# Performance work log

Measured on AMD Instinct MI355X. Metric: run time of the kernel, lower is better.

## Reference

```python
import jax, jax.numpy as jnp
import numpy as np

D = 256      # model_dim
H = 4        # num_heads
DPH = D // H # dim_per_head = 64
NLBL = 9     # number of per-label linear layers


def setup_inputs() -> dict:
    key0 = jax.random.key(0)
    ks = jax.random.split(key0, 16)
    N, M = 6144, 6144
    s = 1.0 / np.sqrt(D)
    inp = {
        'key':     jax.random.normal(ks[0], (N, D), jnp.float32),
        'value':   jax.random.normal(ks[1], (N, D), jnp.float32),
        'query':   jax.random.normal(ks[2], (M, D), jnp.float32),
        'label_1': jax.random.randint(ks[3], (N,), 0, NLBL),
        'label_2': jax.random.randint(ks[4], (M,), 0, NLBL),
        # 9 per-label projection weights (applied as x @ W + b)
        'Wq': jax.random.normal(ks[5], (NLBL, D, D), jnp.float32) * s,
        'bq': jax.random.normal(ks[6], (NLBL, D), jnp.float32) * 0.02,
        'Wk': jax.random.normal(ks[7], (NLBL, D, D), jnp.float32) * s,
        'bk': jax.random.normal(ks[8], (NLBL, D), jnp.float32) * 0.02,
        'Wv': jax.random.normal(ks[9], (NLBL, D, D), jnp.float32) * s,
        'bv': jax.random.normal(ks[10], (NLBL, D), jnp.float32) * 0.02,
        'Wf': jax.random.normal(ks[11], (D, D), jnp.float32) * s,
        'bf': jax.random.normal(ks[12], (D,), jnp.float32) * 0.02,
        'gamma': jnp.ones((D,), jnp.float32),
        'beta':  jnp.zeros((D,), jnp.float32),
    }
    return inp


def _label_proj(x, W, b, lbl):
    # Project every token with all 9 label weights, then pick the per-token one.
    # p: [n, 9, D]
    p = jnp.einsum('nd,ldo->nlo', x, W) + b[None]
    return jnp.take_along_axis(p, lbl[:, None, None], axis=1)[:, 0]  # [n, D]


def reference(key, value, query, label_1, label_2,
              Wq, bq, Wk, bk, Wv, bv, Wf, bf, gamma, beta):
    M = query.shape[0]
    # Per-label (dynamically routed) projections; within a group the query
    # label equals the key label, so per-token weight selection is exactly
    # the per-group loop of the original module.
    q = _label_proj(query, Wq, bq, label_2).reshape(M, H, DPH)
    k = _label_proj(key,   Wk, bk, label_1).reshape(-1, H, DPH)
    v = _label_proj(value, Wv, bv, label_1).reshape(-1, H, DPH)

    # Note: original uses scale = (dim_per_head // num_heads) ** -0.5
    scale = (DPH // H) ** (-0.5)
    scores = jnp.einsum('mhd,nhd->hmn', q, k) * scale  # [H, M, N]

    # Queries only attend to keys of the same label (block structure of
    # the original per-label gather/attention/scatter loop).
    mask = label_2[:, None] == label_1[None, :]        # [M, N]
    probs = jax.nn.softmax(jnp.where(mask[None], scores, -1e30), axis=-1)

    ctx = jnp.einsum('hmn,nhd->mhd', probs, v).reshape(M, D)
    out = ctx @ Wf + bf
    res = query + out  # residual is the unprojected query

    mu = jnp.mean(res, axis=-1, keepdims=True)
    var = jnp.var(res, axis=-1, keepdims=True)
    return (res - mu) / jnp.sqrt(var + 1e-5) * gamma + beta
```

## Files before the change

kernel.cpp:

```cpp
#include <hip/hip_runtime.h>
#include <hip/hip_bf16.h>

#define D 256
#define H 4
#define DPH 64
#define NLBL 9
#define SPLITK 4

typedef __attribute__((ext_vector_type(8))) __bf16 bf16x8;
typedef __attribute__((ext_vector_type(8))) unsigned short u16x8;
typedef __attribute__((ext_vector_type(4))) float f32x4;

__device__ __forceinline__ int sw_idx(int row, int col) {
  return row * 64 + (col ^ ((row & 7) << 3));
}

__device__ __forceinline__ unsigned int pk2(float a, float b) {
  unsigned int lo = (unsigned int)__builtin_bit_cast(unsigned short, (__bf16)a);
  unsigned int hi = (unsigned int)__builtin_bit_cast(unsigned short, (__bf16)b);
  return lo | (hi << 16);
}

__device__ __forceinline__ float b2f(unsigned short u) {
  return __builtin_bit_cast(float, (unsigned int)u << 16);
}

__device__ __forceinline__ bf16x8 cvt8(float4 u0, float4 u1) {
  bf16x8 r;
  r[0] = (__bf16)u0.x; r[1] = (__bf16)u0.y; r[2] = (__bf16)u0.z; r[3] = (__bf16)u0.w;
  r[4] = (__bf16)u1.x; r[5] = (__bf16)u1.y; r[6] = (__bf16)u1.z; r[7] = (__bf16)u1.w;
  return r;
}

__global__ __launch_bounds__(1024) void prep_kernel(
    const int* __restrict__ lbl1, int n1, const int* __restrict__ lbl2, int n2,
    const float* __restrict__ Wq, const float* __restrict__ Wk,
    const float* __restrict__ Wv, const float* __restrict__ Wf,
    __bf16* __restrict__ Wqt, __bf16* __restrict__ Wkt,
    __bf16* __restrict__ Wvt, __bf16* __restrict__ Wft,
    int* __restrict__ cnt, int* __restrict__ off,
    int* __restrict__ pqo, int* __restrict__ pko,
    int* __restrict__ tq, int* __restrict__ tk, int* __restrict__ ntl,
    int* __restrict__ korder, int* __restrict__ qorder) {
  const int job = blockIdx.x;
  const int t = threadIdx.x, lane = t & 63, wave = t >> 6;

  __shared__ int bins[2 * NLBL];
  __shared__ int wtot[16];
  __shared__ float tlds[64][65];

  if (job < 18) {
    const int l = job % NLBL, a = job / NLBL;
    const int n = a ? n2 : n1;
    const int* lbl = a ? lbl2 : lbl1;
    int* order = a ? qorder : korder;

    if (t < NLBL) bins[t] = 0;
    __syncthreads();
    for (int chunk = 0; chunk < n; chunk += 1024) {
      int i = chunk + t;
      int lb = (i < n) ? lbl[i] : -1;
#pragma unroll
      for (int lab = 0; lab < NLBL; ++lab) {
        unsigned long long bal = __ballot(lb == lab);
        if (lane == 0 && bal) atomicAdd(&bins[lab], __popcll(bal));
      }
    }
    __syncthreads();
    int base = 0;
#pragma unroll
    for (int i = 0; i < NLBL; ++i) base += (i < l) ? bins[i] : 0;

    int pos = 0;
    for (int chunk = 0; chunk < n; chunk += 1024) {
      int i = chunk + t;
      bool flag = (i < n) && (lbl[i] == l);
      unsigned long long bal = __ballot(flag);
      int wprefix = __popcll(bal & ((1ull << lane) - 1ull));
      if (lane == 0) wtot[wave] = __popcll(bal);
      __syncthreads();
      int prew = 0, tot = 0;
#pragma unroll
      for (int w = 0; w < 16; ++w) {
        prew += (w < wave) ? wtot[w] : 0;
        tot += wtot[w];
      }
      if (flag) order[base + pos + prew + wprefix] = i;
      pos += tot;
      __syncthreads();
    }
    return;
  }

  if (job == 18) {
    if (t < 2 * NLBL) bins[t] = 0;
    __syncthreads();
    for (int a = 0; a < 2; ++a) {
      const int n = a ? n2 : n1;
      const int* lbl = a ? lbl2 : lbl1;
      for (int chunk = 0; chunk < n; chunk += 1024) {
        int i = chunk + t;
        int lb = (i < n) ? lbl[i] : -1;
#pragma unroll
        for (int lab = 0; lab < NLBL; ++lab) {
          unsigned long long bal = __ballot(lb == lab);
          if (lane == 0 && bal) atomicAdd(&bins[a * NLBL + lab], __popcll(bal));
        }
      }
    }
    __syncthreads();
    if (t < 2 * NLBL) cnt[t] = bins[t];
    if (t == 0) {
      int a0 = 0, a1 = 0, p0 = 0, p1 = 0, t0 = 0, t1 = 0;
      for (int l = 0; l < NLBL; ++l) {
        off[l] = a0;      a0 += bins[l];
        off[10 + l] = a1; a1 += bins[NLBL + l];
        pko[l] = p0; pqo[l] = p1;
        int tkl = (bins[l] + 63) >> 6;
        int tql = (bins[NLBL + l] + 127) >> 7;
        for (int i = 0; i < tkl; ++i) { tk[2 * t0] = l; tk[2 * t0 + 1] = p0 + (i << 6); ++t0; }
        for (int i = 0; i < tql; ++i) { tq[2 * t1] = l; tq[2 * t1 + 1] = p1 + (i << 7); ++t1; }
        p0 += tkl << 6; p1 += tql << 7;
      }
      off[9] = a0; off[19] = a1; pko[9] = p0; pqo[9] = p1;
      ntl[0] = t1; ntl[1] = t0;
    }
    return;
  }

  {
    int j = job - 19;
    int m = j >> 4, sub = j & 15;
    const float* src; __bf16* dst;
    if (m < 9)       { src = Wq + (size_t)m * 65536;        dst = Wqt + (size_t)m * 65536; }
    else if (m < 18) { src = Wk + (size_t)(m - 9) * 65536;  dst = Wkt + (size_t)(m - 9) * 65536; }
    else if (m < 27) { src = Wv + (size_t)(m - 18) * 65536; dst = Wvt + (size_t)(m - 18) * 65536; }
    else             { src = Wf;                            dst = Wft; }
    int k0 = (sub >> 2) << 6, n0 = (sub & 3) << 6;
    int rr = t >> 6, c = t & 63;
#pragma unroll
    for (int i = 0; i < 4; ++i) {
      int r = i * 16 + rr;
      tlds[r][c] = src[(size_t)(k0 + r) * D + n0 + c];
    }
    __syncthreads();
#pragma unroll
    for (int i = 0; i < 4; ++i) {
      int r = i * 16 + rr;
      dst[(size_t)(n0 + r) * D + k0 + c] = (__bf16)tlds[c][r];
    }
  }
}

__global__ __launch_bounds__(256) void gemm_in_kernel(
    const float* __restrict__ query, const float* __restrict__ key,
    const float* __restrict__ value,
    const __bf16* __restrict__ Wqt, const __bf16* __restrict__ Wkt,
    const __bf16* __restrict__ Wvt,
    const float* __restrict__ bq, const float* __restrict__ bk,
    const float* __restrict__ bv,
    const int* __restrict__ qorder, const int* __restrict__ korder,
    const int* __restrict__ off, const int* __restrict__ cnt,
    const int* __restrict__ pqo, const int* __restrict__ pko,
    const int* __restrict__ tq, const int* __restrict__ tk,
    const int* __restrict__ ntl,
    __bf16* __restrict__ qbuf, __bf16* __restrict__ kbuf, __bf16* __restrict__ vbuf) {
  const int y = blockIdx.y;
  const int nt = (y == 0) ? ntl[0] : ntl[1];
  const int ti = (y == 0) ? ((int)blockIdx.x >> 2) : ((int)blockIdx.x >> 1);
  const int sub = (y == 0) ? ((int)blockIdx.x & 3) : ((int)blockIdx.x & 1);
  if (ti >= nt) return;
  const int* tt = (y == 0) ? tq : tk;
  const float* x = (y == 0) ? query : (y == 1 ? key : value);
  const __bf16* W = (y == 0) ? Wqt : (y == 1 ? Wkt : Wvt);
  const float* bias = (y == 0) ? bq : (y == 1 ? bk : bv);
  const int* order = (y == 0) ? qorder : korder;
  const int* po = (y == 0) ? pqo : pko;
  __bf16* outp = (y == 0) ? qbuf : (y == 1 ? kbuf : vbuf);
  const float sc = (y == 0) ? 0.36067376f : 1.0f;

  const int l = tt[2 * ti], prow0 = tt[2 * ti + 1] + sub * 32;
  const int cl = (y == 0) ? cnt[NLBL + l] : cnt[l];
  const int ooff = (y == 0) ? off[10 + l] : off[l];
  const int base = prow0 - po[l];

  const int t = threadIdx.x, w = t >> 6, lane = t & 63;
  const int lr = lane & 15, lk = lane >> 4;

  int src[2];
#pragma unroll
  for (int fi = 0; fi < 2; ++fi) {
    int ridx = base + fi * 16 + lr;
    src[fi] = (ridx < cl) ? order[ooff + ridx] : -1;
  }

  bf16x8 az;
#pragma unroll
  for (int j = 0; j < 8; ++j) az[j] = (__bf16)0.f;

  f32x4 acc[2][4];
#pragma unroll
  for (int i = 0; i < 2; ++i)
#pragma unroll
    for (int j = 0; j < 4; ++j) acc[i][j] = (f32x4){0.f, 0.f, 0.f, 0.f};

  for (int kb = 0; kb < 8; ++kb) {
    const int kbase = kb * 32 + lk * 8;
    bf16x8 a[2], b[4];
#pragma unroll
    for (int fi = 0; fi < 2; ++fi) {
      if (src[fi] >= 0) {
        const float* ap = x + (size_t)src[fi] * D + kbase;
        float4 u0 = *(const float4*)ap;
        float4 u1 = *(const float4*)(ap + 4);
        a[fi] = cvt8(u0, u1);
      } else {
        a[fi] = az;
      }
    }
#pragma unroll
    for (int fj = 0; fj < 4; ++fj) {
      int col = w * 64 + fj * 16 + lr;
      b[fj] = *(const bf16x8*)(W + (size_t)l * 65536 + (size_t)col * D + kbase);
    }
#pragma unroll
    for (int fi = 0; fi < 2; ++fi)
#pragma unroll
      for (int fj = 0; fj < 4; ++fj)
        acc[fi][fj] = __builtin_amdgcn_mfma_f32_16x16x32_bf16(a[fi], b[fj], acc[fi][fj], 0, 0, 0);
  }

#pragma unroll
  for (int fj = 0; fj < 4; ++fj) {
    int col = w * 64 + fj * 16 + lr;
    float bv_ = bias[l * D + col];
#pragma unroll
    for (int fi = 0; fi < 2; ++fi)
#pragma unroll
      for (int r = 0; r < 4; ++r) {
        int row = prow0 + fi * 16 + lk * 4 + r;
        outp[(size_t)row * D + col] = (__bf16)((acc[fi][fj][r] + bv_) * sc);
      }
  }
}

__global__ __launch_bounds__(256) void attn_mfma(
    const __bf16* __restrict__ qbuf, const __bf16* __restrict__ kbuf,
    const __bf16* __restrict__ vbuf, const int* __restrict__ cnt,
    const int* __restrict__ tq, const int* __restrict__ ntl,
    const int* __restrict__ pko,
    __bf16* __restrict__ pctx, float* __restrict__ pstats) {
  const int tqi = blockIdx.x;
  if (tqi >= ntl[0]) return;
  const int l = tq[2 * tqi], prow0 = tq[2 * tqi + 1];
  const int h = blockIdx.y, s = blockIdx.z;
  const int nk = cnt[l];
  const int ntiles = (nk + 63) >> 6;
  const int ntsz = (ntiles + SPLITK - 1) / SPLITK;
  const int tt0 = s * ntsz;
  const int tt1 = min(ntiles, tt0 + ntsz);
  if (tt0 >= tt1) return;

  const int t = threadIdx.x;
  const int w = t >> 6, lane = t & 63;
  const int lr = lane & 15, lk = lane >> 4;

  __shared__ __align__(16) unsigned short ks[4096];
  __shared__ __align__(16) unsigned short vtl[4096];
  __shared__ __align__(16) unsigned short plds[8192];

  const int qbase = prow0 + w * 32;
  bf16x8 b_q[2][2];
#pragma unroll
  for (int qf = 0; qf < 2; ++qf)
#pragma unroll
    for (int kb = 0; kb < 2; ++kb)
      b_q[qf][kb] = *(const bf16x8*)(qbuf + (size_t)(qbase + qf * 16 + lr) * D +
                                     h * DPH + kb * 32 + lk * 8);

  f32x4 acc_o[2][4];
#pragma unroll
  for (int qf = 0; qf < 2; ++qf)
#pragma unroll
    for (int i = 0; i < 4; ++i) acc_o[qf][i] = (f32x4){0.f, 0.f, 0.f, 0.f};
  float lrun[2] = {0.f, 0.f};
  const int kb0 = pko[l];

  const int krow = t >> 2, kc0 = (t & 3) * 16;
  const __bf16* kptr = kbuf + (size_t)(kb0 + krow) * D + h * DPH + kc0;
  const int vkey2 = (t & 31) * 2, vd0 = (t >> 5) * 8;
  const __bf16* vptr = vbuf + (size_t)(kb0 + vkey2) * D + h * DPH + vd0;

  uint4 kreg0, kreg1;
  u16x8 vreg0, vreg1;
  auto LOADT = [&](int tt) {
    const __bf16* kp = kptr + ((size_t)tt << 6) * D;
    kreg0 = *(const uint4*)kp;
    kreg1 = *(const uint4*)(kp + 8);
    const __bf16* vp = vptr + ((size_t)tt << 6) * D;
    vreg0 = *(const u16x8*)vp;
    vreg1 = *(const u16x8*)(vp + D);
  };

  LOADT(tt0);
  for (int tt = tt0; tt < tt1; ++tt) {
    const int n0 = tt << 6;
    __syncthreads();
    *(uint4*)&ks[sw_idx(krow, kc0)] = kreg0;
    *(uint4*)&ks[sw_idx(krow, kc0 + 8)] = kreg1;
#pragma unroll
    for (int j = 0; j < 8; ++j) {
      unsigned int u = (unsigned int)vreg0[j] | ((unsigned int)vreg1[j] << 16);
      *(unsigned int*)&vtl[sw_idx(vd0 + j, vkey2)] = u;
    }
    __syncthreads();
    if (tt + 1 < tt1) LOADT(tt + 1);

    f32x4 s_acc[2][4];
    const f32x4 zz = {0.f, 0.f, 0.f, 0.f};
#pragma unroll
    for (int fi = 0; fi < 4; ++fi) {
      bf16x8 a0 = *(const bf16x8*)&ks[sw_idx(fi * 16 + lr, lk * 8)];
#pragma unroll
      for (int qf = 0; qf < 2; ++qf)
        s_acc[qf][fi] = __builtin_amdgcn_mfma_f32_16x16x32_bf16(a0, b_q[qf][0], zz, 0, 0, 0);
    }
#pragma unroll
    for (int fi = 0; fi < 4; ++fi) {
      bf16x8 a1 = *(const bf16x8*)&ks[sw_idx(fi * 16 + lr, 32 + lk * 8)];
#pragma unroll
      for (int qf = 0; qf < 2; ++qf)
        s_acc[qf][fi] = __builtin_amdgcn_mfma_f32_16x16x32_bf16(a1, b_q[qf][1], s_acc[qf][fi], 0, 0, 0);
    }

    float p[2][16];
#pragma unroll
    for (int qf = 0; qf < 2; ++qf) {
      float ts = 0.f;
#pragma unroll
      for (int fi = 0; fi < 4; ++fi)
#pragma unroll
        for (int r = 0; r < 4; ++r) {
          int key = n0 + fi * 16 + lk * 4 + r;
          float pv = (key < nk) ? exp2f(s_acc[qf][fi][r]) : 0.f;
          p[qf][fi * 4 + r] = pv;
          ts += pv;
        }
      ts += __shfl_xor(ts, 16, 64);
      ts += __shfl_xor(ts, 32, 64);
      lrun[qf] += ts;
    }

#pragma unroll
    for (int qf = 0; qf < 2; ++qf)
#pragma unroll
      for (int fi = 0; fi < 4; ++fi) {
        unsigned int w0 = pk2(p[qf][fi * 4 + 0], p[qf][fi * 4 + 1]);
        unsigned int w1 = pk2(p[qf][fi * 4 + 2], p[qf][fi * 4 + 3]);
        int idx = w * 2048 + sw_idx(qf * 16 + lr, fi * 16 + lk * 4);
        *(uint2*)&plds[idx] = make_uint2(w0, w1);
      }

#pragma unroll
    for (int kb = 0; kb < 2; ++kb) {
      bf16x8 bp[2];
#pragma unroll
      for (int qf = 0; qf < 2; ++qf)
        bp[qf] = *(const bf16x8*)&plds[w * 2048 + sw_idx(qf * 16 + lr, kb * 32 + lk * 8)];
#pragma unroll
      for (int fi = 0; fi < 4; ++fi) {
        bf16x8 av = *(const bf16x8*)&vtl[sw_idx(fi * 16 + lr, kb * 32 + lk * 8)];
#pragma unroll
        for (int qf = 0; qf < 2; ++qf)
          acc_o[qf][fi] = __builtin_amdgcn_mfma_f32_16x16x32_bf16(av, bp[qf], acc_o[qf][fi], 0, 0, 0);
      }
    }
  }

  const size_t pbase = ((size_t)tqi * H + h) * SPLITK + s;
  __bf16* pc = pctx + pbase * 8192;
#pragma unroll
  for (int qf = 0; qf < 2; ++qf) {
    int qloc = w * 32 + qf * 16 + lr;
#pragma unroll
    for (int fi = 0; fi < 4; ++fi) {
      uint2 u;
      u.x = pk2(acc_o[qf][fi][0], acc_o[qf][fi][1]);
      u.y = pk2(acc_o[qf][fi][2], acc_o[qf][fi][3]);
      *(uint2*)(pc + qloc * 64 + fi * 16 + lk * 4) = u;
    }
    if (lk == 0) pstats[pbase * 128 + qloc] = lrun[qf];
  }
}

__global__ __launch_bounds__(256) void proj_ln_kernel(
    const __bf16* __restrict__ pctx, const float* __restrict__ pstats,
    const __bf16* __restrict__ Wft, const float* __restrict__ bf_,
    const float* __restrict__ query,
    const int* __restrict__ qorder, const int* __restrict__ off,
    const int* __restrict__ cnt, const int* __restrict__ pqo,
    const int* __restrict__ tq, const int* __restrict__ ntl,
    const float* __restrict__ gamma, const float* __restrict__ beta,
    float* __restrict__ out) {
  const int tqi = blockIdx.x;
  if (tqi >= ntl[0]) return;
  const int l = tq[2 * tqi];
  const int qq = blockIdx.y;
  const int prow0 = tq[2 * tqi + 1] + qq * 32;
  const int qloc0 = qq * 32;
  const int cl = cnt[NLBL + l];
  const int ooff = off[10 + l];
  const int base = prow0 - pqo[l];
  const int nk = cnt[l];
  const int ntiles = (nk + 63) >> 6;
  const int ntsz = (ntiles + SPLITK - 1) / SPLITK;
  const int nsp = ntiles ? (ntiles + ntsz - 1) / ntsz : 0;

  const int t = threadIdx.x, w = t >> 6, lane = t & 63;
  const int lr = lane & 15, lk = lane >> 4;

  __shared__ int srcs[32];
  __shared__ float linv[32][4];
  __shared__ __align__(16) unsigned short ct[32 * 256];
  __shared__ float psum[4][32], psum2[4][32];
  __shared__ float mu_s[32], is_s[32];

  if (t < 32) {
    int ridx = base + t;
    srcs[t] = (ridx < cl) ? qorder[ooff + ridx] : -1;
  }
  if (t < 128) {
    int row = t >> 2, h = t & 3;
    float L = 0.f;
    for (int s = 0; s < nsp; ++s)
      L += pstats[(((size_t)tqi * H + h) * SPLITK + s) * 128 + qloc0 + row];
    linv[row][h] = (L > 0.f) ? (1.f / L) : 0.f;
  }
  __syncthreads();

  {
    int row = t >> 3, dseg = (t & 7) * 32;
    int h = dseg >> 6, d0 = dseg & 63;
    const __bf16* pb = pctx + (((size_t)tqi * H + h) * SPLITK) * 8192 +
                       (size_t)(qloc0 + row) * 64 + d0;
    float v[32];
#pragma unroll
    for (int j = 0; j < 32; ++j) v[j] = 0.f;
    for (int s = 0; s < nsp; ++s) {
      const __bf16* ps = pb + (size_t)s * 8192;
#pragma unroll
      for (int j4 = 0; j4 < 4; ++j4) {
        u16x8 u = *(const u16x8*)(ps + j4 * 8);
#pragma unroll
        for (int e = 0; e < 8; ++e) v[j4 * 8 + e] += b2f(u[e]);
      }
    }
    float iv = linv[row][h];
    int xr = (row & 7) << 3;
#pragma unroll
    for (int j = 0; j < 32; j += 2)
      *(unsigned int*)&ct[row * 256 + ((dseg + j) ^ xr)] = pk2(v[j] * iv, v[j + 1] * iv);
  }
  __syncthreads();

  f32x4 acc[2][4];
#pragma unroll
  for (int i = 0; i < 2; ++i)
#pragma unroll
    for (int j = 0; j < 4; ++j) acc[i][j] = (f32x4){0.f, 0.f, 0.f, 0.f};

  for (int kb = 0; kb < 8; ++kb) {
    const int kbase = kb * 32 + lk * 8;
    bf16x8 a[2], b[4];
#pragma unroll
    for (int fi = 0; fi < 2; ++fi) {
      int row = fi * 16 + lr;
      a[fi] = *(const bf16x8*)&ct[row * 256 + (kbase ^ ((row & 7) << 3))];
    }
#pragma unroll
    for (int fj = 0; fj < 4; ++fj) {
      int col = w * 64 + fj * 16 + lr;
      b[fj] = *(const bf16x8*)(Wft + (size_t)col * D + kbase);
    }
#pragma unroll
    for (int fi = 0; fi < 2; ++fi)
#pragma unroll
      for (int fj = 0; fj < 4; ++fj)
        acc[fi][fj] = __builtin_amdgcn_mfma_f32_16x16x32_bf16(a[fi], b[fj], acc[fi][fj], 0, 0, 0);
  }

  float res[2][4][4];
  float s1[2][4], s2[2][4];
#pragma unroll
  for (int fi = 0; fi < 2; ++fi)
#pragma unroll
    for (int r = 0; r < 4; ++r) { s1[fi][r] = 0.f; s2[fi][r] = 0.f; }

#pragma unroll
  for (int fj = 0; fj < 4; ++fj) {
    int col = w * 64 + fj * 16 + lr;
    float bcol = bf_[col];
#pragma unroll
    for (int fi = 0; fi < 2; ++fi)
#pragma unroll
      for (int r = 0; r < 4; ++r) {
        int rowl = fi * 16 + lk * 4 + r;
        int sr = srcs[rowl];
        float qv = (sr >= 0) ? query[(size_t)sr * D + col] : 0.f;
        float v = acc[fi][fj][r] + bcol + qv;
        res[fi][fj][r] = v;
        s1[fi][r] += v;
        s2[fi][r] += v * v;
      }
  }

#pragma unroll
  for (int o2 = 1; o2 <= 8; o2 <<= 1) {
#pragma unroll
    for (int fi = 0; fi < 2; ++fi)
#pragma unroll
      for (int r = 0; r < 4; ++r) {
        s1[fi][r] += __shfl_xor(s1[fi][r], o2, 64);
        s2[fi][r] += __shfl_xor(s2[fi][r], o2, 64);
      }
  }
  if (lr == 0) {
#pragma unroll
    for (int fi = 0; fi < 2; ++fi)
#pragma unroll
      for (int r = 0; r < 4; ++r) {
        int rowl = fi * 16 + lk * 4 + r;
        psum[w][rowl] = s1[fi][r];
        psum2[w][rowl] = s2[fi][r];
      }
  }
  __syncthreads();
  if (t < 32) {
    float tot = psum[0][t] + psum[1][t] + psum[2][t] + psum[3][t];
    float tot2 = psum2[0][t] + psum2[1][t] + psum2[2][t] + psum2[3][t];
    float mu = tot * (1.f / D);
    float var = tot2 * (1.f / D) - mu * mu;
    mu_s[t] = mu;
    is_s[t] = rsqrtf(var + 1e-5f);
  }
  __syncthreads();

#pragma unroll
  for (int fj = 0; fj < 4; ++fj) {
    int col = w * 64 + fj * 16 + lr;
    float gc = gamma[col], bc = beta[col];
#pragma unroll
    for (int fi = 0; fi < 2; ++fi)
#pragma unroll
      for (int r = 0; r < 4; ++r) {
        int rowl = fi * 16 + lk * 4 + r;
        int sr = srcs[rowl];
        if (sr >= 0)
          out[(size_t)sr * D + col] =
              (res[fi][fj][r] - mu_s[rowl]) * is_s[rowl] * gc + bc;
      }
  }
}

extern "C" void kernel_launch(void* const* d_in, const int* in_sizes, int n_in,
                              void* d_out, int out_size, void* d_ws, size_t ws_size,
                              hipStream_t stream) {
  const float* key   = (const float*)d_in[0];
  const float* value = (const float*)d_in[1];
  const float* query = (const float*)d_in[2];
  const int*   lbl1  = (const int*)d_in[3];
  const int*   lbl2  = (const int*)d_in[4];
  const float* Wq = (const float*)d_in[5];
  const float* bq = (const float*)d_in[6];
  const float* Wk = (const float*)d_in[7];
  const float* bk = (const float*)d_in[8];
  const float* Wv = (const float*)d_in[9];
  const float* bv = (const float*)d_in[10];
  const float* Wf = (const float*)d_in[11];
  const float* bf_ = (const float*)d_in[12];
  const float* gamma = (const float*)d_in[13];
  const float* beta  = (const float*)d_in[14];
  float* out = (float*)d_out;

  const int N = in_sizes[0] / D;
  const int M = in_sizes[2] / D;
  const int MP = M + NLBL * 128;
  const int NP = N + NLBL * 64;
  const int TQCAP = (M + 127) / 128 + NLBL;
  const int TKCAP = (N + 63) / 64 + NLBL;

  int* cnt = (int*)d_ws;
  int* off = cnt + 32;
  int* pqo = off + 32;
  int* pko = pqo + 16;
  int* ntl = pko + 16;
  int* tq  = ntl + 16;
  int* tk  = tq + 2 * TQCAP;
  int* korder = tk + 2 * TKCAP;
  int* qorder = korder + N;
  size_t ihdr = (((size_t)(112 + 2 * TQCAP + 2 * TKCAP + N + M)) * 4 + 255) & ~(size_t)255;

  __bf16* Wqt = (__bf16*)((char*)d_ws + ihdr);
  __bf16* Wkt = Wqt + (size_t)9 * 65536;
  __bf16* Wvt = Wkt + (size_t)9 * 65536;
  __bf16* Wft = Wvt + (size_t)9 * 65536;
  __bf16* qbuf = Wft + 65536;
  __bf16* kbuf = qbuf + (size_t)MP * D;
  __bf16* vbuf = kbuf + (size_t)NP * D;
  __bf16* pctx = vbuf + (size_t)NP * D;
  float* pstats = (float*)(pctx + (size_t)TQCAP * H * SPLITK * 8192);

  prep_kernel<<<19 + 28 * 16, 1024, 0, stream>>>(
      lbl1, N, lbl2, M, Wq, Wk, Wv, Wf, Wqt, Wkt, Wvt, Wft,
      cnt, off, pqo, pko, tq, tk, ntl, korder, qorder);

  int gx = TQCAP * 4 > TKCAP * 2 ? TQCAP * 4 : TKCAP * 2;
  gemm_in_kernel<<<dim3(gx, 3), 256, 0, stream>>>(
      query, key, value, Wqt, Wkt, Wvt, bq, bk, bv,
      qorder, korder, off, cnt, pqo, pko, tq, tk, ntl, qbuf, kbuf, vbuf);

  attn_mfma<<<dim3(TQCAP, H, SPLITK), 256, 0, stream>>>(
      qbuf, kbuf, vbuf, cnt, tq, ntl, pko, pctx, pstats);

  proj_ln_kernel<<<dim3(TQCAP, 4), 256, 0, stream>>>(
      pctx, pstats, Wft, bf_, query, qorder, off, cnt, pqo, tq, ntl,
      gamma, beta, out);
}
```

Before: 88.92 us.

## Fuse four kernels into one persistent cooperative kernel with grid syncs

Merges the prep, input GEMM, attention and projection+LayerNorm kernels into a single persistent cooperative kernel. Blocks loop over jobs in each phase and phases are separated by grid-wide syncs. The per-kernel launch gaps go away and the grid is sized from occupancy. The prep phase now runs with 256-thread blocks instead of 1024, and shared memory is a union across phases. Grid syncs add overhead, and using fewer blocks than before may reduce parallelism in the attention phase.

```diff
diff --git a/kernel.cpp b/kernel.cpp
--- a/kernel.cpp
+++ b/kernel.cpp
@@ -1,11 +1,16 @@
 #include <hip/hip_runtime.h>
 #include <hip/hip_bf16.h>
+#include <hip/hip_cooperative_groups.h>
+
+namespace cg = cooperative_groups;
 
 #define D 256
 #define H 4
 #define DPH 64
 #define NLBL 9
 #define SPLITK 4
+#define GRID 512
+#define BLK 256
 
 typedef __attribute__((ext_vector_type(8))) __bf16 bf16x8;
 typedef __attribute__((ext_vector_type(8))) unsigned short u16x8;
@@ -32,60 +37,72 @@
   return r;
 }
 
-__global__ __launch_bounds__(1024) void prep_kernel(
-    const int* __restrict__ lbl1, int n1, const int* __restrict__ lbl2, int n2,
-    const float* __restrict__ Wq, const float* __restrict__ Wk,
-    const float* __restrict__ Wv, const float* __restrict__ Wf,
-    __bf16* __restrict__ Wqt, __bf16* __restrict__ Wkt,
-    __bf16* __restrict__ Wvt, __bf16* __restrict__ Wft,
-    int* __restrict__ cnt, int* __restrict__ off,
-    int* __restrict__ pqo, int* __restrict__ pko,
-    int* __restrict__ tq, int* __restrict__ tk, int* __restrict__ ntl,
-    int* __restrict__ korder, int* __restrict__ qorder) {
-  const int job = blockIdx.x;
+struct SMemSC { int bins[2 * NLBL]; int wtot[4]; };
+struct SMemAT { unsigned short ks[4096]; unsigned short vtl[4096]; unsigned short plds[8192]; };
+struct SMemPL {
+  int srcs[32]; float linv[32][4];
+  unsigned short ct[32 * 256];
+  float psum[4][32], psum2[4][32], mu_s[32], is_s[32];
+};
+union __align__(16) SMem {
+  SMemSC sc;
+  float tlds[64][65];
+  SMemAT at;
+  SMemPL pl;
+};
+
+struct P {
+  const float *key, *value, *query;
+  const int *lbl1, *lbl2;
+  const float *Wq, *bq, *Wk, *bk, *Wv, *bv, *Wf, *bf_, *gamma, *beta;
+  float* out;
+  int N, M;
+  int *cnt, *off, *pqo, *pko, *tq, *tk, *ntl, *korder, *qorder;
+  __bf16 *Wqt, *Wkt, *Wvt, *Wft, *qbuf, *kbuf, *vbuf, *pctx;
+  float* pstats;
+  int phase_lo, phase_hi;
+};
+
+__device__ void ph_prep(const P& p, SMem& sm, int job) {
   const int t = threadIdx.x, lane = t & 63, wave = t >> 6;
-
-  __shared__ int bins[2 * NLBL];
-  __shared__ int wtot[16];
-  __shared__ float tlds[64][65];
 
   if (job < 18) {
     const int l = job % NLBL, a = job / NLBL;
-    const int n = a ? n2 : n1;
-    const int* lbl = a ? lbl2 : lbl1;
-    int* order = a ? qorder : korder;
-
-    if (t < NLBL) bins[t] = 0;
+    const int n = a ? p.M : p.N;
+    const int* lbl = a ? p.lbl2 : p.lbl1;
+    int* order = a ? p.qorder : p.korder;
+
+    if (t < NLBL) sm.sc.bins[t] = 0;
     __syncthreads();
-    for (int chunk = 0; chunk < n; chunk += 1024) {
+    for (int chunk = 0; chunk < n; chunk += BLK) {
       int i = chunk + t;
       int lb = (i < n) ? lbl[i] : -1;
 #pragma unroll
       for (int lab = 0; lab < NLBL; ++lab) {
         unsigned long long bal = __ballot(lb == lab);
-        if (lane == 0 && bal) atomicAdd(&bins[lab], __popcll(bal));
+        if (lane == 0 && bal) atomicAdd(&sm.sc.bins[lab], __popcll(bal));
       }
     }
     __syncthreads();
     int base = 0;
 #pragma unroll
-    for (int i = 0; i < NLBL; ++i) base += (i < l) ? bins[i] : 0;
+    for (int i = 0; i < NLBL; ++i) base += (i < l) ? sm.sc.bins[i] : 0;
 
     int pos = 0;
-    for (int chunk = 0; chunk < n; chunk += 1024) {
+    for (int chunk = 0; chunk < n; chunk += BLK) {
       int i = chunk + t;
       bool flag = (i < n) && (lbl[i] == l);
       unsigned long long bal = __ballot(flag);
-      int wprefix = __popcll(bal & ((1ull << lane) - 1ull));
-      if (lane == 0) wtot[wave] = __popcll(bal);
+      int wpref = __popcll(bal & ((1ull << lane) - 1ull));
+      if (lane == 0) sm.sc.wtot[wave] = __popcll(bal);
       __syncthreads();
       int prew = 0, tot = 0;
 #pragma unroll
-      for (int w = 0; w < 16; ++w) {
-        prew += (w < wave) ? wtot[w] : 0;
-        tot += wtot[w];
-      }
-      if (flag) order[base + pos + prew + wprefix] = i;
+      for (int w = 0; w < 4; ++w) {
+        prew += (w < wave) ? sm.sc.wtot[w] : 0;
+        tot += sm.sc.wtot[w];
+      }
+      if (flag) order[base + pos + prew + wpref] = i;
       pos += tot;
       __syncthreads();
     }
@@ -93,37 +110,37 @@
   }
 
   if (job == 18) {
-    if (t < 2 * NLBL) bins[t] = 0;
+    if (t < 2 * NLBL) sm.sc.bins[t] = 0;
     __syncthreads();
     for (int a = 0; a < 2; ++a) {
-      const int n = a ? n2 : n1;
-      const int* lbl = a ? lbl2 : lbl1;
-      for (int chunk = 0; chunk < n; chunk += 1024) {
+      const int n = a ? p.M : p.N;
+      const int* lbl = a ? p.lbl2 : p.lbl1;
+      for (int chunk = 0; chunk < n; chunk += BLK) {
         int i = chunk + t;
         int lb = (i < n) ? lbl[i] : -1;
 #pragma unroll
         for (int lab = 0; lab < NLBL; ++lab) {
           unsigned long long bal = __ballot(lb == lab);
-          if (lane == 0 && bal) atomicAdd(&bins[a * NLBL + lab], __popcll(bal));
+          if (lane == 0 && bal) atomicAdd(&sm.sc.bins[a * NLBL + lab], __popcll(bal));
         }
       }
     }
     __syncthreads();
-    if (t < 2 * NLBL) cnt[t] = bins[t];
+    if (t < 2 * NLBL) p.cnt[t] = sm.sc.bins[t];
     if (t == 0) {
       int a0 = 0, a1 = 0, p0 = 0, p1 = 0, t0 = 0, t1 = 0;
       for (int l = 0; l < NLBL; ++l) {
-        off[l] = a0;      a0 += bins[l];
-        off[10 + l] = a1; a1 += bins[NLBL + l];
-        pko[l] = p0; pqo[l] = p1;
-        int tkl = (bins[l] + 63) >> 6;
-        int tql = (bins[NLBL + l] + 127) >> 7;
-        for (int i = 0; i < tkl; ++i) { tk[2 * t0] = l; tk[2 * t0 + 1] = p0 + (i << 6); ++t0; }
-        for (int i = 0; i < tql; ++i) { tq[2 * t1] = l; tq[2 * t1 + 1] = p1 + (i << 7); ++t1; }
+        p.off[l] = a0;      a0 += sm.sc.bins[l];
+        p.off[10 + l] = a1; a1 += sm.sc.bins[NLBL + l];
+        p.pko[l] = p0; p.pqo[l] = p1;
+        int tkl = (sm.sc.bins[l] + 63) >> 6;
+        int tql = (sm.sc.bins[NLBL + l] + 127) >> 7;
+        for (int i = 0; i < tkl; ++i) { p.tk[2 * t0] = l; p.tk[2 * t0 + 1] = p0 + (i << 6); ++t0; }
+        for (int i = 0; i < tql; ++i) { p.tq[2 * t1] = l; p.tq[2 * t1 + 1] = p1 + (i << 7); ++t1; }
         p0 += tkl << 6; p1 += tql << 7;
       }
-      off[9] = a0; off[19] = a1; pko[9] = p0; pqo[9] = p1;
-      ntl[0] = t1; ntl[1] = t0;
+      p.off[9] = a0; p.off[19] = a1; p.pko[9] = p0; p.pqo[9] = p1;
+      p.ntl[0] = t1; p.ntl[1] = t0;
     }
     return;
   }
@@ -132,56 +149,39 @@
     int j = job - 19;
     int m = j >> 4, sub = j & 15;
     const float* src; __bf16* dst;
-    if (m < 9)       { src = Wq + (size_t)m * 65536;        dst = Wqt + (size_t)m * 65536; }
-    else if (m < 18) { src = Wk + (size_t)(m - 9) * 65536;  dst = Wkt + (size_t)(m - 9) * 65536; }
-    else if (m < 27) { src = Wv + (size_t)(m - 18) * 65536; dst = Wvt + (size_t)(m - 18) * 65536; }
-    else             { src = Wf;                            dst = Wft; }
+    if (m < 9)       { src = p.Wq + (size_t)m * 65536;        dst = p.Wqt + (size_t)m * 65536; }
+    else if (m < 18) { src = p.Wk + (size_t)(m - 9) * 65536;  dst = p.Wkt + (size_t)(m - 9) * 65536; }
+    else if (m < 27) { src = p.Wv + (size_t)(m - 18) * 65536; dst = p.Wvt + (size_t)(m - 18) * 65536; }
+    else             { src = p.Wf;                            dst = p.Wft; }
     int k0 = (sub >> 2) << 6, n0 = (sub & 3) << 6;
     int rr = t >> 6, c = t & 63;
 #pragma unroll
-    for (int i = 0; i < 4; ++i) {
-      int r = i * 16 + rr;
-      tlds[r][c] = src[(size_t)(k0 + r) * D + n0 + c];
+    for (int i = 0; i < 16; ++i) {
+      int r = i * 4 + rr;
+      sm.tlds[r][c] = src[(size_t)(k0 + r) * D + n0 + c];
     }
     __syncthreads();
 #pragma unroll
-    for (int i = 0; i < 4; ++i) {
-      int r = i * 16 + rr;
-      dst[(size_t)(n0 + r) * D + k0 + c] = (__bf16)tlds[c][r];
-    }
-  }
-}
-
-__global__ __launch_bounds__(256) void gemm_in_kernel(
-    const float* __restrict__ query, const float* __restrict__ key,
-    const float* __restrict__ value,
-    const __bf16* __restrict__ Wqt, const __bf16* __restrict__ Wkt,
-    const __bf16* __restrict__ Wvt,
-    const float* __restrict__ bq, const float* __restrict__ bk,
-    const float* __restrict__ bv,
-    const int* __restrict__ qorder, const int* __restrict__ korder,
-    const int* __restrict__ off, const int* __restrict__ cnt,
-    const int* __restrict__ pqo, const int* __restrict__ pko,
-    const int* __restrict__ tq, const int* __restrict__ tk,
-    const int* __restrict__ ntl,
-    __bf16* __restrict__ qbuf, __bf16* __restrict__ kbuf, __bf16* __restrict__ vbuf) {
-  const int y = blockIdx.y;
-  const int nt = (y == 0) ? ntl[0] : ntl[1];
-  const int ti = (y == 0) ? ((int)blockIdx.x >> 2) : ((int)blockIdx.x >> 1);
-  const int sub = (y == 0) ? ((int)blockIdx.x & 3) : ((int)blockIdx.x & 1);
-  if (ti >= nt) return;
-  const int* tt = (y == 0) ? tq : tk;
-  const float* x = (y == 0) ? query : (y == 1 ? key : value);
-  const __bf16* W = (y == 0) ? Wqt : (y == 1 ? Wkt : Wvt);
-  const float* bias = (y == 0) ? bq : (y == 1 ? bk : bv);
-  const int* order = (y == 0) ? qorder : korder;
-  const int* po = (y == 0) ? pqo : pko;
-  __bf16* outp = (y == 0) ? qbuf : (y == 1 ? kbuf : vbuf);
+    for (int i = 0; i < 16; ++i) {
+      int r = i * 4 + rr;
+      dst[(size_t)(n0 + r) * D + k0 + c] = (__bf16)sm.tlds[c][r];
+    }
+  }
+}
+
+__device__ void ph_gemm(const P& p, int y, int ti, int sub) {
+  const int* tt = (y == 0) ? p.tq : p.tk;
+  const float* x = (y == 0) ? p.query : (y == 1 ? p.key : p.value);
+  const __bf16* W = (y == 0) ? p.Wqt : (y == 1 ? p.Wkt : p.Wvt);
+  const float* bias = (y == 0) ? p.bq : (y == 1 ? p.bk : p.bv);
+  const int* order = (y == 0) ? p.qorder : p.korder;
+  const int* po = (y == 0) ? p.pqo : p.pko;
+  __bf16* outp = (y == 0) ? p.qbuf : (y == 1 ? p.kbuf : p.vbuf);
   const float sc = (y == 0) ? 0.36067376f : 1.0f;
 
   const int l = tt[2 * ti], prow0 = tt[2 * ti + 1] + sub * 32;
-  const int cl = (y == 0) ? cnt[NLBL + l] : cnt[l];
-  const int ooff = (y == 0) ? off[10 + l] : off[l];
+  const int cl = (y == 0) ? p.cnt[NLBL + l] : p.cnt[l];
+  const int ooff = (y == 0) ? p.off[10 + l] : p.off[l];
   const int base = prow0 - po[l];
 
   const int t = threadIdx.x, w = t >> 6, lane = t & 63;
@@ -244,17 +244,9 @@
   }
 }
 
-__global__ __launch_bounds__(256) void attn_mfma(
-    const __bf16* __restrict__ qbuf, const __bf16* __restrict__ kbuf,
-    const __bf16* __restrict__ vbuf, const int* __restrict__ cnt,
-    const int* __restrict__ tq, const int* __restrict__ ntl,
-    const int* __restrict__ pko,
-    __bf16* __restrict__ pctx, float* __restrict__ pstats) {
-  const int tqi = blockIdx.x;
-  if (tqi >= ntl[0]) return;
-  const int l = tq[2 * tqi], prow0 = tq[2 * tqi + 1];
-  const int h = blockIdx.y, s = blockIdx.z;
-  const int nk = cnt[l];
+__device__ void ph_attn(const P& p, SMem& sm, int tqi, int h, int s) {
+  const int l = p.tq[2 * tqi], prow0 = p.tq[2 * tqi + 1];
+  const int nk = p.cnt[l];
   const int ntiles = (nk + 63) >> 6;
   const int ntsz = (ntiles + SPLITK - 1) / SPLITK;
   const int tt0 = s * ntsz;
@@ -265,17 +257,13 @@
   const int w = t >> 6, lane = t & 63;
   const int lr = lane & 15, lk = lane >> 4;
 
-  __shared__ __align__(16) unsigned short ks[4096];
-  __shared__ __align__(16) unsigned short vtl[4096];
-  __shared__ __align__(16) unsigned short plds[8192];
-
   const int qbase = prow0 + w * 32;
   bf16x8 b_q[2][2];
 #pragma unroll
   for (int qf = 0; qf < 2; ++qf)
 #pragma unroll
     for (int kb = 0; kb < 2; ++kb)
-      b_q[qf][kb] = *(const bf16x8*)(qbuf + (size_t)(qbase + qf * 16 + lr) * D +
+      b_q[qf][kb] = *(const bf16x8*)(p.qbuf + (size_t)(qbase + qf * 16 + lr) * D +
                                      h * DPH + kb * 32 + lk * 8);
 
   f32x4 acc_o[2][4];
@@ -284,12 +272,12 @@
 #pragma unroll
     for (int i = 0; i < 4; ++i) acc_o[qf][i] = (f32x4){0.f, 0.f, 0.f, 0.f};
   float lrun[2] = {0.f, 0.f};
-  const int kb0 = pko[l];
+  const int kb0 = p.pko[l];
 
   const int krow = t >> 2, kc0 = (t & 3) * 16;
-  const __bf16* kptr = kbuf + (size_t)(kb0 + krow) * D + h * DPH + kc0;
+  const __bf16* kptr = p.kbuf + (size_t)(kb0 + krow) * D + h * DPH + kc0;
   const int vkey2 = (t & 31) * 2, vd0 = (t >> 5) * 8;
-  const __bf16* vptr = vbuf + (size_t)(kb0 + vkey2) * D + h * DPH + vd0;
+  const __bf16* vptr = p.vbuf + (size_t)(kb0 + vkey2) * D + h * DPH + vd0;
 
   uint4 kreg0, kreg1;
   u16x8 vreg0, vreg1;
@@ -306,12 +294,12 @@
   for (int tt = tt0; tt < tt1; ++tt) {
     const int n0 = tt << 6;
     __syncthreads();
-    *(uint4*)&ks[sw_idx(krow, kc0)] = kreg0;
-    *(uint4*)&ks[sw_idx(krow, kc0 + 8)] = kreg1;
+    *(uint4*)&sm.at.ks[sw_idx(krow, kc0)] = kreg0;
+    *(uint4*)&sm.at.ks[sw_idx(krow, kc0 + 8)] = kreg1;
 #pragma unroll
     for (int j = 0; j < 8; ++j) {
       unsigned int u = (unsigned int)vreg0[j] | ((unsigned int)vreg1[j] << 16);
-      *(unsigned int*)&vtl[sw_idx(vd0 + j, vkey2)] = u;
+      *(unsigned int*)&sm.at.vtl[sw_idx(vd0 + j, vkey2)] = u;
     }
     __syncthreads();
     if (tt + 1 < tt1) LOADT(tt + 1);
@@ -320,20 +308,20 @@
     const f32x4 zz = {0.f, 0.f, 0.f, 0.f};
 #pragma unroll
     for (int fi = 0; fi < 4; ++fi) {
-      bf16x8 a0 = *(const bf16x8*)&ks[sw_idx(fi * 16 + lr, lk * 8)];
+      bf16x8 a0 = *(const bf16x8*)&sm.at.ks[sw_idx(fi * 16 + lr, lk * 8)];
 #pragma unroll
       for (int qf = 0; qf < 2; ++qf)
         s_acc[qf][fi] = __builtin_amdgcn_mfma_f32_16x16x32_bf16(a0, b_q[qf][0], zz, 0, 0, 0);
     }
 #pragma unroll
     for (int fi = 0; fi < 4; ++fi) {
-      bf16x8 a1 = *(const bf16x8*)&ks[sw_idx(fi * 16 + lr, 32 + lk * 8)];
+      bf16x8 a1 = *(const bf16x8*)&sm.at.ks[sw_idx(fi * 16 + lr, 32 + lk * 8)];
 #pragma unroll
       for (int qf = 0; qf < 2; ++qf)
         s_acc[qf][fi] = __builtin_amdgcn_mfma_f32_16x16x32_bf16(a1, b_q[qf][1], s_acc[qf][fi], 0, 0, 0);
     }
 
-    float p[2][16];
+    float pw[2][16];
 #pragma unroll
     for (int qf = 0; qf < 2; ++qf) {
       float ts = 0.f;
@@ -343,7 +331,7 @@
         for (int r = 0; r < 4; ++r) {
           int key = n0 + fi * 16 + lk * 4 + r;
           float pv = (key < nk) ? exp2f(s_acc[qf][fi][r]) : 0.f;
-          p[qf][fi * 4 + r] = pv;
+          pw[qf][fi * 4 + r] = pv;
           ts += pv;
         }
       ts += __shfl_xor(ts, 16, 64);
@@ -355,10 +343,10 @@
     for (int qf = 0; qf < 2; ++qf)
 #pragma unroll
       for (int fi = 0; fi < 4; ++fi) {
-        unsigned int w0 = pk2(p[qf][fi * 4 + 0], p[qf][fi * 4 + 1]);
-        unsigned int w1 = pk2(p[qf][fi * 4 + 2], p[qf][fi * 4 + 3]);
+        unsigned int w0 = pk2(pw[qf][fi * 4 + 0], pw[qf][fi * 4 + 1]);
+        unsigned int w1 = pk2(pw[qf][fi * 4 + 2], pw[qf][fi * 4 + 3]);
         int idx = w * 2048 + sw_idx(qf * 16 + lr, fi * 16 + lk * 4);
-        *(uint2*)&plds[idx] = make_uint2(w0, w1);
+        *(uint2*)&sm.at.plds[idx] = make_uint2(w0, w1);
       }
 
 #pragma unroll
@@ -366,10 +354,10 @@
       bf16x8 bp[2];
 #pragma unroll
       for (int qf = 0; qf < 2; ++qf)
-        bp[qf] = *(const bf16x8*)&plds[w * 2048 + sw_idx(qf * 16 + lr, kb * 32 + lk * 8)];
+        bp[qf] = *(const bf16x8*)&sm.at.plds[w * 2048 + sw_idx(qf * 16 + lr, kb * 32 + lk * 8)];
 #pragma unroll
       for (int fi = 0; fi < 4; ++fi) {
-        bf16x8 av = *(const bf16x8*)&vtl[sw_idx(fi * 16 + lr, kb * 32 + lk * 8)];
+        bf16x8 av = *(const bf16x8*)&sm.at.vtl[sw_idx(fi * 16 + lr, kb * 32 + lk * 8)];
 #pragma unroll
         for (int qf = 0; qf < 2; ++qf)
           acc_o[qf][fi] = __builtin_amdgcn_mfma_f32_16x16x32_bf16(av, bp[qf], acc_o[qf][fi], 0, 0, 0);
@@ -378,7 +366,7 @@
   }
 
   const size_t pbase = ((size_t)tqi * H + h) * SPLITK + s;
-  __bf16* pc = pctx + pbase * 8192;
+  __bf16* pc = p.pctx + pbase * 8192;
 #pragma unroll
   for (int qf = 0; qf < 2; ++qf) {
     int qloc = w * 32 + qf * 16 + lr;
@@ -389,29 +377,18 @@
       u.y = pk2(acc_o[qf][fi][2], acc_o[qf][fi][3]);
       *(uint2*)(pc + qloc * 64 + fi * 16 + lk * 4) = u;
     }
-    if (lk == 0) pstats[pbase * 128 + qloc] = lrun[qf];
-  }
-}
-
-__global__ __launch_bounds__(256) void proj_ln_kernel(
-    const __bf16* __restrict__ pctx, const float* __restrict__ pstats,
-    const __bf16* __restrict__ Wft, const float* __restrict__ bf_,
-    const float* __restrict__ query,
-    const int* __restrict__ qorder, const int* __restrict__ off,
-    const int* __restrict__ cnt, const int* __restrict__ pqo,
-    const int* __restrict__ tq, const int* __restrict__ ntl,
-    const float* __restrict__ gamma, const float* __restrict__ beta,
-    float* __restrict__ out) {
-  const int tqi = blockIdx.x;
-  if (tqi >= ntl[0]) return;
-  const int l = tq[2 * tqi];
-  const int qq = blockIdx.y;
-  const int prow0 = tq[2 * tqi + 1] + qq * 32;
+    if (lk == 0) p.pstats[pbase * 128 + qloc] = lrun[qf];
+  }
+}
+
+__device__ void ph_proj(const P& p, SMem& sm, int tqi, int qq) {
+  const int l = p.tq[2 * tqi];
+  const int prow0 = p.tq[2 * tqi + 1] + qq * 32;
   const int qloc0 = qq * 32;
-  const int cl = cnt[NLBL + l];
-  const int ooff = off[10 + l];
-  const int base = prow0 - pqo[l];
-  const int nk = cnt[l];
+  const int cl = p.cnt[NLBL + l];
+  const int ooff = p.off[10 + l];
+  const int base = prow0 - p.pqo[l];
+  const int nk = p.cnt[l];
   const int ntiles = (nk + 63) >> 6;
   const int ntsz = (ntiles + SPLITK - 1) / SPLITK;
   const int nsp = ntiles ? (ntiles + ntsz - 1) / ntsz : 0;
@@ -419,29 +396,23 @@
   const int t = threadIdx.x, w = t >> 6, lane = t & 63;
   const int lr = lane & 15, lk = lane >> 4;
 
-  __shared__ int srcs[32];
-  __shared__ float linv[32][4];
-  __shared__ __align__(16) unsigned short ct[32 * 256];
-  __shared__ float psum[4][32], psum2[4][32];
-  __shared__ float mu_s[32], is_s[32];
-
   if (t < 32) {
     int ridx = base + t;
-    srcs[t] = (ridx < cl) ? qorder[ooff + ridx] : -1;
+    sm.pl.srcs[t] = (ridx < cl) ? p.qorder[ooff + ridx] : -1;
   }
   if (t < 128) {
     int row = t >> 2, h = t & 3;
     float L = 0.f;
     for (int s = 0; s < nsp; ++s)
-      L += pstats[(((size_t)tqi * H + h) * SPLITK + s) * 128 + qloc0 + row];
-    linv[row][h] = (L > 0.f) ? (1.f / L) : 0.f;
+      L += p.pstats[(((size_t)tqi * H + h) * SPLITK + s) * 128 + qloc0 + row];
+    sm.pl.linv[row][h] = (L > 0.f) ? (1.f / L) : 0.f;
   }
   __syncthreads();
 
   {
     int row = t >> 3, dseg = (t & 7) * 32;
     int h = dseg >> 6, d0 = dseg & 63;
-    const __bf16* pb = pctx + (((size_t)tqi * H + h) * SPLITK) * 8192 +
+    const __bf16* pb = p.pctx + (((size_t)tqi * H + h) * SPLITK) * 8192 +
                        (size_t)(qloc0 + row) * 64 + d0;
     float v[32];
 #pragma unroll
@@ -455,11 +426,11 @@
         for (int e = 0; e < 8; ++e) v[j4 * 8 + e] += b2f(u[e]);
       }
     }
-    float iv = linv[row][h];
+    float iv = sm.pl.linv[row][h];
     int xr = (row & 7) << 3;
 #pragma unroll
     for (int j = 0; j < 32; j += 2)
-      *(unsigned int*)&ct[row * 256 + ((dseg + j) ^ xr)] = pk2(v[j] * iv, v[j + 1] * iv);
+      *(unsigned int*)&sm.pl.ct[row * 256 + ((dseg + j) ^ xr)] = pk2(v[j] * iv, v[j + 1] * iv);
   }
   __syncthreads();
 
@@ -475,12 +446,12 @@
 #pragma unroll
     for (int fi = 0; fi < 2; ++fi) {
       int row = fi * 16 + lr;
-      a[fi] = *(const bf16x8*)&ct[row * 256 + (kbase ^ ((row & 7) << 3))];
+      a[fi] = *(const bf16x8*)&sm.pl.ct[row * 256 + (kbase ^ ((row & 7) << 3))];
     }
 #pragma unroll
     for (int fj = 0; fj < 4; ++fj) {
       int col = w * 64 + fj * 16 + lr;
-      b[fj] = *(const bf16x8*)(Wft + (size_t)col * D + kbase);
+      b[fj] = *(const bf16x8*)(p.Wft + (size_t)col * D + kbase);
     }
 #pragma unroll
     for (int fi = 0; fi < 2; ++fi)
@@ -499,14 +470,14 @@
 #pragma unroll
   for (int fj = 0; fj < 4; ++fj) {
     int col = w * 64 + fj * 16 + lr;
-    float bcol = bf_[col];
+    float bcol = p.bf_[col];
 #pragma unroll
     for (int fi = 0; fi < 2; ++fi)
 #pragma unroll
       for (int r = 0; r < 4; ++r) {
         int rowl = fi * 16 + lk * 4 + r;
-        int sr = srcs[rowl];
-        float qv = (sr >= 0) ? query[(size_t)sr * D + col] : 0.f;
+        int sr = sm.pl.srcs[rowl];
+        float qv = (sr >= 0) ? p.query[(size_t)sr * D + col] : 0.f;
         float v = acc[fi][fj][r] + bcol + qv;
         res[fi][fj][r] = v;
         s1[fi][r] += v;
@@ -530,99 +501,150 @@
 #pragma unroll
       for (int r = 0; r < 4; ++r) {
         int rowl = fi * 16 + lk * 4 + r;
-        psum[w][rowl] = s1[fi][r];
-        psum2[w][rowl] = s2[fi][r];
+        sm.pl.psum[w][rowl] = s1[fi][r];
+        sm.pl.psum2[w][rowl] = s2[fi][r];
       }
   }
   __syncthreads();
   if (t < 32) {
-    float tot = psum[0][t] + psum[1][t] + psum[2][t] + psum[3][t];
-    float tot2 = psum2[0][t] + psum2[1][t] + psum2[2][t] + psum2[3][t];
+    float tot = sm.pl.psum[0][t] + sm.pl.psum[1][t] + sm.pl.psum[2][t] + sm.pl.psum[3][t];
+    float tot2 = sm.pl.psum2[0][t] + sm.pl.psum2[1][t] + sm.pl.psum2[2][t] + sm.pl.psum2[3][t];
     float mu = tot * (1.f / D);
     float var = tot2 * (1.f / D) - mu * mu;
-    mu_s[t] = mu;
-    is_s[t] = rsqrtf(var + 1e-5f);
+    sm.pl.mu_s[t] = mu;
+    sm.pl.is_s[t] = rsqrtf(var + 1e-5f);
   }
   __syncthreads();
 
 #pragma unroll
   for (int fj = 0; fj < 4; ++fj) {
     int col = w * 64 + fj * 16 + lr;
-    float gc = gamma[col], bc = beta[col];
+    float gc = p.gamma[col], bc = p.beta[col];
 #pragma unroll
     for (int fi = 0; fi < 2; ++fi)
 #pragma unroll
       for (int r = 0; r < 4; ++r) {
         int rowl = fi * 16 + lk * 4 + r;
-        int sr = srcs[rowl];
+        int sr = sm.pl.srcs[rowl];
         if (sr >= 0)
-          out[(size_t)sr * D + col] =
-              (res[fi][fj][r] - mu_s[rowl]) * is_s[rowl] * gc + bc;
-      }
+          p.out[(size_t)sr * D + col] =
+              (res[fi][fj][r] - sm.pl.mu_s[rowl]) * sm.pl.is_s[rowl] * gc + bc;
+      }
+  }
+}
+
+__global__ __launch_bounds__(BLK, 2) void mega(P p) {
+  __shared__ SMem sm;
+  cg::grid_group grid = cg::this_grid();
+
+  for (int ph = p.phase_lo; ph <= p.phase_hi; ++ph) {
+    int njobs;
+    int ntq = 0, ntk = 0;
+    if (ph == 0) njobs = 19 + 28 * 16;
+    else {
+      ntq = p.ntl[0]; ntk = p.ntl[1];
+      njobs = (ph == 1) ? (ntq * 4 + ntk * 4)
+            : (ph == 2) ? (ntq * H * SPLITK)
+                        : (ntq * 4);
+    }
+    for (int job = blockIdx.x; job < njobs; job += gridDim.x) {
+      __syncthreads();
+      if (ph == 0) {
+        ph_prep(p, sm, job);
+      } else if (ph == 1) {
+        int n0 = ntq * 4, n1 = n0 + ntk * 2;
+        int y, ti, sub;
+        if (job < n0)      { y = 0; ti = job >> 2; sub = job & 3; }
+        else if (job < n1) { int j = job - n0; y = 1; ti = j >> 1; sub = j & 1; }
+        else               { int j = job - n1; y = 2; ti = j >> 1; sub = j & 1; }
+        ph_gemm(p, y, ti, sub);
+      } else if (ph == 2) {
+        ph_attn(p, sm, job >> 4, (job >> 2) & 3, job & 3);
+      } else {
+        ph_proj(p, sm, job >> 2, job & 3);
+      }
+    }
+    if (ph < p.phase_hi) {
+      __threadfence();
+      grid.sync();
+    }
   }
 }
 
 extern "C" void kernel_launch(void* const* d_in, const int* in_sizes, int n_in,
                               void* d_out, int out_size, void* d_ws, size_t ws_size,
                               hipStream_t stream) {
-  const float* key   = (const float*)d_in[0];
-  const float* value = (const float*)d_in[1];
-  const float* query = (const float*)d_in[2];
-  const int*   lbl1  = (const int*)d_in[3];
-  const int*   lbl2  = (const int*)d_in[4];
-  const float* Wq = (const float*)d_in[5];
-  const float* bq = (const float*)d_in[6];
-  const float* Wk = (const float*)d_in[7];
-  const float* bk = (const float*)d_in[8];
-  const float* Wv = (const float*)d_in[9];
-  const float* bv = (const float*)d_in[10];
-  const float* Wf = (const float*)d_in[11];
-  const float* bf_ = (const float*)d_in[12];
-  const float* gamma = (const float*)d_in[13];
-  const float* beta  = (const float*)d_in[14];
-  float* out = (float*)d_out;
-
   const int N = in_sizes[0] / D;
   const int M = in_sizes[2] / D;
+  const int TQCAP = (M + 127) / 128 + NLBL;
+  const int TKCAP = (N + 63) / 64 + NLBL;
+
+  P p;
+  p.key   = (const float*)d_in[0];
+  p.value = (const float*)d_in[1];
+  p.query = (const float*)d_in[2];
+  p.lbl1  = (const int*)d_in[3];
+  p.lbl2  = (const int*)d_in[4];
+  p.Wq = (const float*)d_in[5];
+  p.bq = (const float*)d_in[6];
+  p.Wk = (const float*)d_in[7];
+  p.bk = (const float*)d_in[8];
+  p.Wv = (const float*)d_in[9];
+  p.bv = (const float*)d_in[10];
+  p.Wf = (const float*)d_in[11];
+  p.bf_ = (const float*)d_in[12];
+  p.gamma = (const float*)d_in[13];
+  p.beta  = (const float*)d_in[14];
+  p.out = (float*)d_out;
+  p.N = N; p.M = M;
+
   const int MP = M + NLBL * 128;
   const int NP = N + NLBL * 64;
-  const int TQCAP = (M + 127) / 128 + NLBL;
-  const int TKCAP = (N + 63) / 64 + NLBL;
-
-  int* cnt = (int*)d_ws;
-  int* off = cnt + 32;
-  int* pqo = off + 32;
-  int* pko = pqo + 16;
-  int* ntl = pko + 16;
-  int* tq  = ntl + 16;
-  int* tk  = tq + 2 * TQCAP;
-  int* korder = tk + 2 * TKCAP;
-  int* qorder = korder + N;
+
+  p.cnt = (int*)d_ws;
+  p.off = p.cnt + 32;
+  p.pqo = p.off + 32;
+  p.pko = p.pqo + 16;
+  p.ntl = p.pko + 16;
+  p.tq  = p.ntl + 16;
+  p.tk  = p.tq + 2 * TQCAP;
+  p.korder = p.tk + 2 * TKCAP;
+  p.qorder = p.korder + N;
   size_t ihdr = (((size_t)(112 + 2 * TQCAP + 2 * TKCAP + N + M)) * 4 + 255) & ~(size_t)255;
 
-  __bf16* Wqt = (__bf16*)((char*)d_ws + ihdr);
-  __bf16* Wkt = Wqt + (size_t)9 * 65536;
-  __bf16* Wvt = Wkt + (size_t)9 * 65536;
-  __bf16* Wft = Wvt + (size_t)9 * 65536;
-  __bf16* qbuf = Wft + 65536;
-  __bf16* kbuf = qbuf + (size_t)MP * D;
-  __bf16* vbuf = kbuf + (size_t)NP * D;
-  __bf16* pctx = vbuf + (size_t)NP * D;
-  float* pstats = (float*)(pctx + (size_t)TQCAP * H * SPLITK * 8192);
-
-  prep_kernel<<<19 + 28 * 16, 1024, 0, stream>>>(
-      lbl1, N, lbl2, M, Wq, Wk, Wv, Wf, Wqt, Wkt, Wvt, Wft,
-      cnt, off, pqo, pko, tq, tk, ntl, korder, qorder);
-
-  int gx = TQCAP * 4 > TKCAP * 2 ? TQCAP * 4 : TKCAP * 2;
-  gemm_in_kernel<<<dim3(gx, 3), 256, 0, stream>>>(
-      query, key, value, Wqt, Wkt, Wvt, bq, bk, bv,
-      qorder, korder, off, cnt, pqo, pko, tq, tk, ntl, qbuf, kbuf, vbuf);
-
-  attn_mfma<<<dim3(TQCAP, H, SPLITK), 256, 0, stream>>>(
-      qbuf, kbuf, vbuf, cnt, tq, ntl, pko, pctx, pstats);
-
-  proj_ln_kernel<<<dim3(TQCAP, 4), 256, 0, stream>>>(
-      pctx, pstats, Wft, bf_, query, qorder, off, cnt, pqo, tq, ntl,
-      gamma, beta, out);
-}
+  p.Wqt = (__bf16*)((char*)d_ws + ihdr);
+  p.Wkt = p.Wqt + (size_t)9 * 65536;
+  p.Wvt = p.Wkt + (size_t)9 * 65536;
+  p.Wft = p.Wvt + (size_t)9 * 65536;
+  p.qbuf = p.Wft + 65536;
+  p.kbuf = p.qbuf + (size_t)MP * D;
+  p.vbuf = p.kbuf + (size_t)NP * D;
+  p.pctx = p.vbuf + (size_t)NP * D;
+  p.pstats = (float*)(p.pctx + (size_t)TQCAP * H * SPLITK * 8192);
+
+  int occ = 0;
+  hipError_t qe = hipOccupancyMaxActiveBlocksPerMultiprocessor(
+      &occ, reinterpret_cast<const void*>(&mega), BLK, 0);
+
+  bool coop_ok = false;
+  if (qe == hipSuccess && occ >= 1) {
+    int grid = occ * 256;
+    if (grid > GRID) grid = GRID;
+    p.phase_lo = 0; p.phase_hi = 3;
+    void* kargs[] = {&p};
+    hipError_t e = hipLaunchCooperativeKernel(
+        reinterpret_cast<const void*>(&mega), dim3(grid), dim3(BLK), kargs, 0, stream);
+    if (e == hipSuccess) coop_ok = true;
+    else (void)hipGetLastError();
+  } else {
+    (void)hipGetLastError();
+  }
+
+  if (!coop_ok) {
+    for (int ph = 0; ph < 4; ++ph) {
+      P q = p;
+      q.phase_lo = ph; q.phase_hi = ph;
+      mega<<<dim3(GRID), dim3(BLK), 0, stream>>>(q);
+    }
+  }
+}
```

Result: slower. 311.2 us (+249.9%).
